# Performance work log

Hardware: AMD Instinct MI355X
Metric: run time of the kernel (lower is better)

The kernel has to match this reference:

```python
import jax, jax.numpy as jnp
import numpy as np

# QMon (monDEQ, Winston & Kolter): conv pre-net -> MONSingleConv + MONBorderReLU solved
# with Peaceman-Rachford splitting -> border crop -> MLP head.
BATCH = 256
C = 64            # DEQ channels
N = 9             # DEQ spatial dim (in_dim=9)
K = 3             # MONSingleConv kernel size
M_STRONG = 0.1    # m (strong monotonicity)
ALPHA = 1.0
TOL = 1e-5
MAX_ITER = 50
OUT_FEATURES = 18


def conv2d(x, w, b=None, stride=1):
    y = jax.lax.conv_general_dilated(x, w, (stride, stride), 'VALID',
                                     dimension_numbers=('NCHW', 'OIHW', 'NCHW'))
    if b is not None:
        y = y + b[None, :, None, None]
    return y


def circ_conv(x, w, b=None):
    # circular-padded 'same' conv (cpad + valid conv in the torch code)
    p = (w.shape[2] - 1) // 2
    xp = jnp.pad(x, ((0, 0), (0, 0), (p, p), (p, p)), mode='wrap')
    return conv2d(xp, w, b)


def circ_conv_T(x, w):
    # adjoint of circular conv = circular conv with spatially-flipped, channel-transposed kernel
    wt = jnp.transpose(jnp.flip(w, (2, 3)), (1, 0, 2, 3))
    return circ_conv(x, wt)


def W_multiply(z, A_w, g):
    # W z = (1-m) z - g * A^T A z, with A Frobenius-normalized
    An = A_w / jnp.linalg.norm(A_w)
    Az = circ_conv(z, An)
    ATAz = circ_conv_T(Az, An)
    return (1.0 - M_STRONG) * z - g * ATAz


def build_inverse(A_w, g, n):
    # ((1+alpha) I - alpha W)^{-1} per 2D-DFT frequency (circular conv is block-circulant)
    An = A_w / jnp.linalg.norm(A_w)
    co, ci, k, _ = An.shape
    p = (k - 1) // 2
    kimg = jnp.zeros((co, ci, n, n), An.dtype)
    for dx in range(k):
        for dy in range(k):
            kimg = kimg.at[:, :, (dx - p) % n, (dy - p) % n].set(An[:, :, dx, dy])
    Af = jnp.conj(jnp.fft.fft2(kimg)).transpose(2, 3, 0, 1)  # (n,n,O,I): A_hat(w)
    I = jnp.eye(co, dtype=Af.dtype)
    c = (1.0 + ALPHA) - ALPHA * (1.0 - M_STRONG)
    Mmat = c * I + (ALPHA * g).astype(Af.dtype) * jnp.einsum('xyoi,xyoj->xyij', jnp.conj(Af), Af)
    return jnp.linalg.inv(Mmat)  # (n,n,C,C) complex


def apply_inverse(Vinv, z):
    zf = jnp.fft.fft2(z)                                  # (B,C,n,n)
    yf = jnp.einsum('xyoc,bcxy->boxy', Vinv, zf)
    return jnp.real(jnp.fft.ifft2(yf)).astype(z.dtype)


def mon_deq(xpre, U_w, U_b, A_w, g):
    n = xpre.shape[-1]
    bias = circ_conv(xpre, U_w, U_b)
    Vinv = build_inverse(A_w, g, n)
    mask = jnp.pad(jnp.ones((n - 2, n - 2), xpre.dtype), 1)[None, None]  # MONBorderReLU border=1
    brelu = lambda v: jax.nn.relu(v) * mask
    z0 = jnp.zeros_like(bias)

    def body(state):
        z, u, err, it = state
        u12 = 2.0 * z - u
        z12 = apply_inverse(Vinv, u12 + ALPHA * bias)
        un = 2.0 * z12 - u12
        zn = brelu(un)
        err = jnp.linalg.norm(zn - z) / (1e-6 + jnp.linalg.norm(zn))
        return zn, un, err, it + 1

    def cond(state):
        _, _, err, it = state
        return (err > TOL) & (it < MAX_ITER)

    z, u, err, it = jax.lax.while_loop(cond, body, (z0, z0, jnp.asarray(1.0, xpre.dtype), 0))
    # final pass with the linear operator (as in the torch forward after the no_grad solve)
    return brelu(W_multiply(z, A_w, g) + bias)


def setup_inputs() -> dict:
    key = jax.random.key(0)
    ks = jax.random.split(key, 12)

    def u(k, shape, fan_in):
        b = 1.0 / np.sqrt(fan_in)
        return jax.random.uniform(k, shape, jnp.float32, -b, b)

    x = jax.random.uniform(ks[0], (BATCH, 4, 84, 84), jnp.float32) * 255.0
    return dict(
        x=x,
        conv1_w=u(ks[1], (32, 4, 8, 8), 4 * 8 * 8), conv1_b=u(ks[2], (32,), 4 * 8 * 8),
        conv2_w=u(ks[3], (64, 32, 4, 4), 32 * 4 * 4), conv2_b=u(ks[4], (64,), 32 * 4 * 4),
        U_w=u(ks[5], (C, C, K, K), C * K * K), U_b=u(ks[6], (C,), C * K * K),
        A_w=u(ks[7], (C, C, K, K), C * K * K), g=jnp.asarray(1.0, jnp.float32),
        fc1_w=u(ks[8], (512, 3136), 3136), fc1_b=u(ks[9], (512,), 3136),
        fc2_w=u(ks[10], (OUT_FEATURES, 512), 512), fc2_b=u(ks[11], (OUT_FEATURES,), 512),
    )


def reference(x, conv1_w, conv1_b, conv2_w, conv2_b, U_w, U_b, A_w, g,
              fc1_w, fc1_b, fc2_w, fc2_b):
    h = jax.nn.relu(conv2d(x / 255.0, conv1_w, conv1_b, stride=4))   # (B,32,20,20)
    h = jax.nn.relu(conv2d(h, conv2_w, conv2_b, stride=2))           # (B,64,9,9)
    z = mon_deq(h, U_w, U_b, A_w, g)                                 # (B,64,9,9)
    z = z[:, :, 1:-1, 1:-1].reshape(z.shape[0], -1)                  # (B,3136)
    h = jax.nn.relu(z @ fc1_w.T + fc1_b)
    return h @ fc2_w.T + fc2_b
```

## Files before the change

### kernel.cpp

```cpp
#include <hip/hip_runtime.h>


#define NB 256
#define NCH 64
#define NP 81
#define NIMG (NB*NCH)
#define MAXIT 50
#define NCAN 41
__device__ __host__ inline int CAN2(int l) {
    return (l < 5) ? l*9 : ((l-5)%9)*9 + ((l-5)/9 + 1);
}

constexpr float C9[9] = {
  1.0f, 0.76604444311897803f, 0.17364817766693041f, -0.5f,
  -0.93969262078590843f, -0.93969262078590843f, -0.5f,
  0.17364817766693041f, 0.76604444311897803f };
constexpr float S9[9] = {
  0.0f, 0.64278760968653936f, 0.98480775301220802f, 0.86602540378443871f,
  0.34202014332566877f, -0.34202014332566877f, -0.86602540378443871f,
  -0.98480775301220802f, -0.64278760968653936f };

__constant__ float COS9[9] = {
  1.0f, 0.76604444311897803f, 0.17364817766693041f, -0.5f,
  -0.93969262078590843f, -0.93969262078590843f, -0.5f,
  0.17364817766693041f, 0.76604444311897803f };
__constant__ float SIN9[9] = {
  0.0f, 0.64278760968653936f, 0.98480775301220802f, 0.86602540378443871f,
  0.34202014332566877f, -0.34202014332566877f, -0.86602540378443871f,
  -0.98480775301220802f, -0.64278760968653936f };

__global__ __launch_bounds__(256) void k_norm(const float* __restrict__ Aw,
                                              float* __restrict__ sc) {
    __shared__ float red[256];
    float s = 0.f;
    for (int i = threadIdx.x; i < 64*64*9; i += 256) { float a = Aw[i]; s += a*a; }
    red[threadIdx.x] = s; __syncthreads();
    for (int w = 128; w > 0; w >>= 1) {
        if (threadIdx.x < w) red[threadIdx.x] += red[threadIdx.x + w];
        __syncthreads();
    }
    if (threadIdx.x == 0) { float n = sqrtf(red[0]); sc[0] = n; sc[1] = 1.f/n; }
}

__global__ __launch_bounds__(512, 4) void k_conv1(const float* __restrict__ x,
                                                  const float* __restrict__ w,
                                                  const float* __restrict__ bb,
                                                  float* __restrict__ y) {
    __shared__ float xl[7056];
    int blk = blockIdx.x, tid = threadIdx.x;
    int b = blk >> 1, og = (blk & 1) << 4;
    float acc[16];
    #pragma unroll
    for (int o = 0; o < 16; ++o) acc[o] = 0.f;
    int p = tid, oy = p/20, ox = p%20;
    for (int ci = 0; ci < 4; ++ci) {
        __syncthreads();
        const float4* xg = (const float4*)(x + b*28224 + ci*7056);
        for (int i = tid; i < 1764; i += 512) ((float4*)xl)[i] = xg[i];
        __syncthreads();
        if (p < 400) {
            #pragma unroll
            for (int ky = 0; ky < 8; ++ky) {
                const float* xr = xl + (oy*4+ky)*84 + ox*4;
                float4 x0 = *(const float4*)xr;
                float4 x1 = *(const float4*)(xr+4);
                const float* wr = w + og*256 + ci*64 + ky*8;
                #pragma unroll
                for (int o = 0; o < 16; ++o) {
                    const float* wo = wr + o*256;
                    acc[o] += x0.x*wo[0] + x0.y*wo[1] + x0.z*wo[2] + x0.w*wo[3]
                            + x1.x*wo[4] + x1.y*wo[5] + x1.z*wo[6] + x1.w*wo[7];
                }
            }
        }
    }
    if (p < 400) {
        #pragma unroll
        for (int o = 0; o < 16; ++o)
            y[b*12800 + (og+o)*400 + p] = fmaxf(acc[o]*(1.f/255.f) + bb[og+o], 0.f);
    }
}

__global__ __launch_bounds__(512, 2) void k_conv2(const float* __restrict__ h1,
                                                  const float* __restrict__ w2,
                                                  const float* __restrict__ b2,
                                                  float* __restrict__ h2) {
    int blk = blockIdx.x, tid = threadIdx.x;
    int b = blk >> 2, og = (blk & 3) << 4;
    __shared__ float hl[16*400];
    __shared__ float wl[16*512];
    for (int i = tid; i < 8192; i += 512) wl[i] = w2[og*512 + i];
    float a0[2], a1[2];
    #pragma unroll
    for (int s = 0; s < 2; ++s) { a0[s] = 0.f; a1[s] = 0.f; }
    for (int cp = 0; cp < 2; ++cp) {
        __syncthreads();
        for (int i = tid; i < 6400; i += 512) {
            int ci = i / 400, pix = i % 400, iy = pix / 20, ix = pix % 20;
            hl[ci*400 + ((iy&1)*2 + (ix&1))*100 + (iy>>1)*10 + (ix>>1)]
                = h1[b*12800 + (cp*16 + ci)*400 + pix];
        }
        __syncthreads();
        #pragma unroll
        for (int s = 0; s < 2; ++s) {
            int idx = tid + s*512;
            if (idx < 648) {
                int op = idx/81, p = idx%81;
                int oy = p/9, ox = p%9;
                int toff[16];
                #pragma unroll
                for (int ky = 0; ky < 4; ky++)
                #pragma unroll
                for (int kx = 0; kx < 4; kx++)
                    toff[ky*4+kx] = ((ky&1)*2 + (kx&1))*100
                                  + (oy + (ky>>1))*10 + (ox + (kx>>1));
                const float* w0 = wl + op*2*512 + cp*256;
                for (int ci = 0; ci < 16; ci++) {
                    float t[16];
                    const float* base = hl + ci*400;
                    #pragma unroll
                    for (int q = 0; q < 16; ++q) t[q] = base[toff[q]];
                    const float* wb0 = w0 + ci*16;
                    const float* wb1 = w0 + 512 + ci*16;
                    #pragma unroll
                    for (int q = 0; q < 16; ++q) {
                        a0[s] += t[q]*wb0[q]; a1[s] += t[q]*wb1[q];
                    }
                }
            }
        }
    }
    #pragma unroll
    for (int s = 0; s < 2; ++s) {
        int idx = tid + s*512;
        if (idx < 648) {
            int op = idx/81, p = idx%81;
            int o = og + op*2;
            h2[b*5184 + o*81 + p]     = fmaxf(a0[s] + b2[o],   0.f);
            h2[b*5184 + (o+1)*81 + p] = fmaxf(a1[s] + b2[o+1], 0.f);
        }
    }
}

__global__ __launch_bounds__(512, 2) void k_bias(const float* __restrict__ h2,
                                                 const float* __restrict__ Uw,
                                                 const float* __restrict__ Ub,
                                                 float* __restrict__ biasT) {
    int blk = blockIdx.x, tid = threadIdx.x;
    int b = blk >> 2, og = (blk & 3) << 4;
    __shared__ float h2l[5184];
    __shared__ float wl[16*576];
    __shared__ float bt[1296];
    for (int i = tid; i < 5184; i += 512) h2l[i] = h2[b*5184 + i];
    for (int i = tid; i < 9216; i += 512) wl[i] = Uw[og*576 + i];
    __syncthreads();
    for (int idx = tid; idx < 648; idx += 512) {
        int op = idx/81, p = idx%81;
        int i0 = p/9, j0 = p%9;
        int im = (i0+8)%9, ip = (i0+1)%9, jm = (j0+8)%9, jp = (j0+1)%9;
        int toff[9] = { im*9+jm, im*9+j0, im*9+jp,
                        i0*9+jm, i0*9+j0, i0*9+jp,
                        ip*9+jm, ip*9+j0, ip*9+jp };
        float a0 = 0.f, a1 = 0.f;
        const float* w0 = wl + op*2*576;
        for (int ci = 0; ci < 64; ci++) {
            float t[9];
            const float* hb = h2l + ci*81;
            #pragma unroll
            for (int q = 0; q < 9; ++q) t[q] = hb[toff[q]];
            const float* wb0 = w0 + ci*9;
            const float* wb1 = w0 + 576 + ci*9;
            #pragma unroll
            for (int q = 0; q < 9; ++q) { a0 += t[q]*wb0[q]; a1 += t[q]*wb1[q]; }
        }
        bt[(op*2)*81 + p]   = a0 + Ub[og + op*2];
        bt[(op*2+1)*81 + p] = a1 + Ub[og + op*2 + 1];
    }
    __syncthreads();
    for (int idx = tid; idx < 1296; idx += 512) {
        int p2 = idx >> 4, o16 = idx & 15;
        biasT[p2*NIMG + b*64 + og + o16] = bt[o16*81 + p2];
    }
}

__global__ __launch_bounds__(256) void k_af(const float* __restrict__ Aw,
                                            const float* __restrict__ sc,
                                            float2* __restrict__ Af) {
    int l = blockIdx.x; int f = CAN2(l);
    int x = f/9, y = f%9;
    float inv = sc[1];
    for (int pr = threadIdx.x; pr < 4096; pr += 256) {
        const float* a = Aw + pr*9;
        float re = 0.f, im = 0.f;
        #pragma unroll
        for (int dx = 0; dx < 3; dx++)
        #pragma unroll
        for (int dy = 0; dy < 3; dy++) {
            int tt = (x*(dx+8) + y*(dy+8)) % 9;
            float v = a[dx*3+dy] * inv;
            re += v * COS9[tt]; im += v * SIN9[tt];
        }
        Af[f*4096 + pr] = make_float2(re, im);
    }
}

__global__ __launch_bounds__(256) void k_mw(const float2* __restrict__ Af,
                                            const float* __restrict__ gp,
                                            float2* __restrict__ Mmat,
                                            float2* __restrict__ WmT) {
    int l = blockIdx.x >> 2, q = blockIdx.x & 3;
    int f = CAN2(l);
    float g = gp[0];
    __shared__ float2 Al[4096];
    for (int i = threadIdx.x; i < 4096; i += 256) Al[i] = Af[f*4096 + i];
    __syncthreads();
    int e = q*1024 + threadIdx.x;
    #pragma unroll
    for (int rep = 0; rep < 4; ++rep, e += 256) {
        int i = e >> 6, j = e & 63;
        float sr = 0.f, si = 0.f;
        for (int o = 0; o < 64; o++) {
            float2 a = Al[o*64 + i], b = Al[o*64 + j];
            sr += a.x*b.x + a.y*b.y;
            si += a.x*b.y - a.y*b.x;
        }
        Mmat[f*4096 + e] = make_float2((i==j ? 1.1f : 0.f) + g*sr, g*si);
        WmT [f*4096 + j*64 + i] = make_float2((i==j ? 0.9f : 0.f) - g*sr, -g*si);
    }
}

__global__ __launch_bounds__(512, 1) void k_inv(float2* __restrict__ Mio) {
    int f = CAN2((int)blockIdx.x);
    __shared__ float2 Mt[64*65];
    __shared__ float2 rowk[2][64];
    __shared__ float2 fcol[2][64];
    int tid = threadIdx.x;
    int i = tid & 63, jg = tid >> 6;
    float2* Mg = Mio + f*4096;
    for (int e = tid; e < 4096; e += 512) Mt[(e>>6)*65 + (e&63)] = Mg[e];
    __syncthreads();
    float2 r[8];
    #pragma unroll
    for (int jj = 0; jj < 8; ++jj) r[jj] = Mt[i*65 + jg*8 + jj];

    for (int k = 0; k < 64; ++k) {
        int buf = k & 1;
        if (i == k) {
            #pragma unroll
            for (int jj = 0; jj < 8; ++jj) rowk[buf][jg*8 + jj] = r[jj];
        }
        if (jg == (k >> 3)) {
            int sel = k & 7;
            float2 v = r[0];
            #pragma unroll
            for (int jj = 1; jj < 8; ++jj) v = (sel == jj) ? r[jj] : v;
            fcol[buf][i] = v;
        }
        __syncthreads();
        float2 d = rowk[buf][k];
        float den = 1.f / (d.x*d.x + d.y*d.y);
        float pr = d.x*den, pi = -d.y*den;
        float2 fi = fcol[buf][i];
        bool piv = (i == k);
        #pragma unroll
        for (int jj = 0; jj < 8; ++jj) {
            int j = jg*8 + jj;
            float2 rw = rowk[buf][j];
            float2 rkj = (j == k) ? make_float2(pr, pi)
                                  : make_float2(rw.x*pr - rw.y*pi,
                                                rw.x*pi + rw.y*pr);
            if (piv) {
                r[jj] = rkj;
            } else {
                float bx = (j == k) ? 0.f : r[jj].x;
                float by = (j == k) ? 0.f : r[jj].y;
                r[jj] = make_float2(bx - (fi.x*rkj.x - fi.y*rkj.y),
                                    by - (fi.x*rkj.y + fi.y*rkj.x));
            }
        }
    }
    __syncthreads();
    #pragma unroll
    for (int jj = 0; jj < 8; ++jj) Mt[(jg*8 + jj)*65 + i] = r[jj];
    __syncthreads();
    for (int e = tid; e < 4096; e += 512) Mg[e] = Mt[(e>>6)*65 + (e&63)];
}

__global__ __launch_bounds__(320) void k_fft(const float* __restrict__ biasT,
                                             float2* __restrict__ Tf) {
    __shared__ float2 T1[9*5*64];
    int lane = threadIdx.x & 63, j = threadIdx.x >> 6;
    int gimg = blockIdx.x*64 + lane;
    for (int r = j; r < 9; r += 5) {
        float tn[9];
        #pragma unroll
        for (int xc = 0; xc < 9; ++xc) tn[xc] = biasT[(r*9 + xc)*NIMG + gimg];
        #pragma unroll
        for (int ky = 0; ky < 5; ++ky) {
            float sr = 0.f, si = 0.f;
            #pragma unroll
            for (int xx = 0; xx < 9; ++xx) {
                const int m = (ky*xx) % 9;
                sr += tn[xx]*C9[m];
                si -= tn[xx]*S9[m];
            }
            T1[(r*5 + ky)*64 + lane] = make_float2(sr, si);
        }
    }
    __syncthreads();
    {
        int ky = j;
        float2 s[9];
        #pragma unroll
        for (int r = 0; r < 9; ++r) s[r] = T1[(r*5 + ky)*64 + lane];
        #pragma unroll
        for (int kx = 0; kx < 9; ++kx) {
            if (kx < 5 || ky > 0) {
                float fr = 0.f, fi = 0.f;
                #pragma unroll
                for (int r = 0; r < 9; ++r) {
                    const int m = (kx*r) % 9;
                    fr += s[r].x*C9[m] + s[r].y*S9[m];
                    fi += s[r].y*C9[m] - s[r].x*S9[m];
                }
                Tf[(kx*9 + ky)*NIMG + gimg] = make_float2(fr, fi);
            }
        }
    }
}

__global__ __launch_bounds__(256) void k_mv(const float2* __restrict__ Tf,
                                            float2* __restrict__ Yf,
                                            const float2* __restrict__ V) {
    int l = blockIdx.x >> 4, bc = blockIdx.x & 15;
    int f = CAN2(l);
    int lane = threadIdx.x & 63;
    int wid  = __builtin_amdgcn_readfirstlane((int)(threadIdx.x >> 6));
    int b0 = bc*16 + wid*4;
    const float2* Vg = V + f*4096 + lane;
    const float2* Tg = Tf + f*NIMG + b0*64;
    float2 a0 = make_float2(0.f,0.f), a1 = a0, a2 = a0, a3 = a0;
    #pragma unroll 8
    for (int c = 0; c < 64; ++c) {
        float2 v = Vg[c*64];
        float2 t0 = Tg[c], t1 = Tg[64+c], t2 = Tg[128+c], t3 = Tg[192+c];
        a0.x += v.x*t0.x - v.y*t0.y; a0.y += v.x*t0.y + v.y*t0.x;
        a1.x += v.x*t1.x - v.y*t1.y; a1.y += v.x*t1.y + v.y*t1.x;
        a2.x += v.x*t2.x - v.y*t2.y; a2.y += v.x*t2.y + v.y*t2.x;
        a3.x += v.x*t3.x - v.y*t3.y; a3.y += v.x*t3.y + v.y*t3.x;
    }
    float2* Yg = Yf + f*NIMG + b0*64 + lane;
    Yg[0] = a0; Yg[64] = a1; Yg[128] = a2; Yg[192] = a3;
}

__global__ __launch_bounds__(640) void k_fuse(const float2* __restrict__ Yf,
                                              float* __restrict__ u12T,
                                              const float* __restrict__ biasT,
                                              float2* __restrict__ Tf,
                                              int last) {
    __shared__ float2 T1[9*5*64];
    int lane = threadIdx.x & 63, j = threadIdx.x >> 6;
    int gimg = blockIdx.x*64 + lane;
    {
        int ky = j >> 1;
        float2 y[9];
        #pragma unroll
        for (int kx = 0; kx < 9; ++kx) {
            int fc; bool cj;
            if (ky == 0 && kx >= 5) { fc = (9 - kx)*9; cj = true; }
            else                    { fc = kx*9 + ky;  cj = false; }
            float2 a = Yf[fc*NIMG + gimg];
            y[kx] = make_float2(a.x, cj ? -a.y : a.y);
        }
        if ((j & 1) == 0) {
            #pragma unroll
            for (int r = 0; r < 5; ++r) {
                float sr = 0.f, si = 0.f;
                #pragma unroll
                for (int kx = 0; kx < 9; ++kx) {
                    const int m = (r*kx) % 9;
                    sr += y[kx].x*C9[m] - y[kx].y*S9[m];
                    si += y[kx].x*S9[m] + y[kx].y*C9[m];
                }
                T1[(r*5 + ky)*64 + lane] = make_float2(sr, si);
            }
        } else {
            #pragma unroll
            for (int r = 5; r < 9; ++r) {
                float sr = 0.f, si = 0.f;
                #pragma unroll
                for (int kx = 0; kx < 9; ++kx) {
                    const int m = (r*kx) % 9;
                    sr += y[kx].x*C9[m] - y[kx].y*S9[m];
                    si += y[kx].x*S9[m] + y[kx].y*C9[m];
                }
                T1[(r*5 + ky)*64 + lane] = make_float2(sr, si);
            }
        }
    }
    __syncthreads();
    if (j < 9) {
        int r = j;
        float2 t1[5];
        #pragma unroll
        for (int ky = 0; ky < 5; ++ky) t1[ky] = T1[(r*5 + ky)*64 + lane];
        float tn[9];
        #pragma unroll
        for (int xc = 0; xc < 9; ++xc) {
            float yr = t1[0].x;
            #pragma unroll
            for (int ky = 1; ky < 5; ++ky) {
                const int m = (xc*ky) % 9;
                yr += 2.f*(t1[ky].x*C9[m] - t1[ky].y*S9[m]);
            }
            yr *= (1.f/81.f);
            int gi = (r*9 + xc)*NIMG + gimg;
            float u12v = u12T[gi];
            float un = 2.f*yr - u12v;
            bool interior = (r >= 1 && r <= 7 && xc >= 1 && xc <= 7);
            float zn = interior ? fmaxf(un, 0.f) : 0.f;
            float u12n = 2.f*zn - un;
            u12T[gi] = u12n;
            tn[xc] = last ? zn : (u12n + biasT[gi]);
        }
        #pragma unroll
        for (int ky = 0; ky < 5; ++ky) {
            float sr = 0.f, si = 0.f;
            #pragma unroll
            for (int xx = 0; xx < 9; ++xx) {
                const int m = (ky*xx) % 9;
                sr += tn[xx]*C9[m];
                si -= tn[xx]*S9[m];
            }
            T1[(r*5 + ky)*64 + lane] = make_float2(sr, si);
        }
    }
    __syncthreads();
    {
        int ky = j >> 1;
        float2 s[9];
        #pragma unroll
        for (int rr = 0; rr < 9; ++rr) s[rr] = T1[(rr*5 + ky)*64 + lane];
        if ((j & 1) == 0) {
            #pragma unroll
            for (int kx = 0; kx < 5; ++kx) {
                float fr = 0.f, fi = 0.f;
                #pragma unroll
                for (int rr = 0; rr < 9; ++rr) {
                    const int m = (kx*rr) % 9;
                    fr += s[rr].x*C9[m] + s[rr].y*S9[m];
                    fi += s[rr].y*C9[m] - s[rr].x*S9[m];
                }
                Tf[(kx*9 + ky)*NIMG + gimg] = make_float2(fr, fi);
            }
        } else if (ky > 0) {
            #pragma unroll
            for (int kx = 5; kx < 9; ++kx) {
                float fr = 0.f, fi = 0.f;
                #pragma unroll
                for (int rr = 0; rr < 9; ++rr) {
                    const int m = (kx*rr) % 9;
                    fr += s[rr].x*C9[m] + s[rr].y*S9[m];
                    fi += s[rr].y*C9[m] - s[rr].x*S9[m];
                }
                Tf[(kx*9 + ky)*NIMG + gimg] = make_float2(fr, fi);
            }
        }
    }
}

__global__ __launch_bounds__(320) void k_crop(const float2* __restrict__ Yf,
                                              const float* __restrict__ biasT,
                                              float* __restrict__ zc) {
    __shared__ float2 T1[9*5*64];
    int lane = threadIdx.x & 63, j = threadIdx.x >> 6;
    int gimg = blockIdx.x*64 + lane;
    {
        int ky = j;
        float2 y[9];
        #pragma unroll
        for (int kx = 0; kx < 9; ++kx) {
            int fc; bool cj;
            if (ky == 0 && kx >= 5) { fc = (9 - kx)*9; cj = true; }
            else                    { fc = kx*9 + ky;  cj = false; }
            float2 a = Yf[fc*NIMG + gimg];
            y[kx] = make_float2(a.x, cj ? -a.y : a.y);
        }
        #pragma unroll
        for (int r = 0; r < 9; ++r) {
            float sr = 0.f, si = 0.f;
            #pragma unroll
            for (int kx = 0; kx < 9; ++kx) {
                const int m = (r*kx) % 9;
                sr += y[kx].x*C9[m] - y[kx].y*S9[m];
                si += y[kx].x*S9[m] + y[kx].y*C9[m];
            }
            T1[(r*5 + ky)*64 + lane] = make_float2(sr, si);
        }
    }
    __syncthreads();
    for (int r = 1 + j; r <= 7; r += 5) {
        float2 t1[5];
        #pragma unroll
        for (int ky = 0; ky < 5; ++ky) t1[ky] = T1[(r*5 + ky)*64 + lane];
        float* zr = zc + (gimg >> 6)*3136 + (gimg & 63)*49 + (r-1)*7;
        #pragma unroll
        for (int xc = 1; xc < 8; ++xc) {
            float yr = t1[0].x;
            #pragma unroll
            for (int ky = 1; ky < 5; ++ky) {
                const int m = (xc*ky) % 9;
                yr += 2.f*(t1[ky].x*C9[m] - t1[ky].y*S9[m]);
            }
            yr *= (1.f/81.f);
            zr[xc-1] = fmaxf(yr + biasT[(r*9 + xc)*NIMG + gimg], 0.f);
        }
    }
}

__global__ __launch_bounds__(256) void k_fc1(const float* __restrict__ A,
                                             const float* __restrict__ W,
                                             const float* __restrict__ bb,
                                             float* __restrict__ H) {
    int bt = blockIdx.x >> 5, ot = blockIdx.x & 31;
    int b0 = bt*16, o0 = ot*16;
    __shared__ float At[16][65], Bt[16][65];
    int tid = threadIdx.x;
    int row = tid >> 6, col = tid & 63;
    int tb = tid >> 4, to = tid & 15;
    float acc = 0.f;
    for (int k0 = 0; k0 < 3136; k0 += 64) {
        #pragma unroll
        for (int s = 0; s < 4; s++) {
            int rr = row + s*4;
            At[rr][col] = A[(b0+rr)*3136 + k0 + col];
            Bt[rr][col] = W[(o0+rr)*3136 + k0 + col];
        }
        __syncthreads();
        #pragma unroll
        for (int kk = 0; kk < 64; kk++)
            acc += At[tb][kk] * Bt[to][kk];
        __syncthreads();
    }
    H[(b0+tb)*512 + o0+to] = fmaxf(acc + bb[o0+to], 0.f);
}

__global__ __launch_bounds__(256) void k_fc2(const float* __restrict__ H,
                                             const float* __restrict__ W,
                                             const float* __restrict__ bb,
                                             float* __restrict__ out) {
    int idx = blockIdx.x*256 + threadIdx.x;
    if (idx >= 4608) return;
    int b = idx/18, o = idx%18;
    const float* h = H + b*512;
    const float* w = W + o*512;
    float acc = 0.f;
    for (int k = 0; k < 512; k++) acc += h[k]*w[k];
    out[idx] = acc + bb[o];
}

extern "C" void kernel_launch(void* const* d_in, const int* in_sizes, int n_in,
                              void* d_out, int out_size, void* d_ws, size_t ws_size,
                              hipStream_t stream) {
    (void)in_sizes; (void)n_in; (void)out_size; (void)ws_size;
    const float* x   = (const float*)d_in[0];
    const float* c1w = (const float*)d_in[1];
    const float* c1b = (const float*)d_in[2];
    const float* c2w = (const float*)d_in[3];
    const float* c2b = (const float*)d_in[4];
    const float* Uw  = (const float*)d_in[5];
    const float* Ub  = (const float*)d_in[6];
    const float* Aw  = (const float*)d_in[7];
    const float* gp  = (const float*)d_in[8];
    const float* f1w = (const float*)d_in[9];
    const float* f1b = (const float*)d_in[10];
    const float* f2w = (const float*)d_in[11];
    const float* f2b = (const float*)d_in[12];

    float* ws = (float*)d_ws;
    float*  h1    = ws + 0;
    float2* Tf    = (float2*)(ws + 0);
    float*  biasT = ws + 3276800;
    float*  u12T  = ws + 4603904;
    float2* Yf    = (float2*)(ws + 5931008);
    float2* Af    = (float2*)(ws + 8585216);
    float2* Minv  = (float2*)(ws + 9248768);
    float2* WmT   = (float2*)(ws + 9912320);
    float*  zc    = ws + 10575872;
    float*  hfc   = ws + 11378688;
    float*  sc    = ws + 11509760;
    float*  h2    = ws + 11509764;

    hipMemsetAsync(u12T, 0, (size_t)1327104*sizeof(float), stream);

    k_norm <<<1,     256, 0, stream>>>(Aw, sc);
    k_conv1<<<512,   512, 0, stream>>>(x, c1w, c1b, h1);
    k_conv2<<<1024,  512, 0, stream>>>(h1, c2w, c2b, h2);
    k_bias <<<1024,  512, 0, stream>>>(h2, Uw, Ub, biasT);
    k_af   <<<NCAN,  256, 0, stream>>>(Aw, sc, Af);
    k_mw   <<<NCAN*4,256, 0, stream>>>(Af, gp, Minv, WmT);
    k_inv  <<<NCAN,  512, 0, stream>>>(Minv);

    k_fft<<<256, 320, 0, stream>>>(biasT, Tf);
    for (int it = 0; it < MAXIT; it++) {
        k_mv  <<<NCAN*16, 256, 0, stream>>>(Tf, Yf, Minv);
        k_fuse<<<256,     640, 0, stream>>>(Yf, u12T, biasT, Tf, it == MAXIT-1);
    }
    k_mv  <<<NCAN*16, 256, 0, stream>>>(Tf, Yf, WmT);
    k_crop<<<256,     320, 0, stream>>>(Yf, biasT, zc);

    k_fc1<<<512, 256, 0, stream>>>(zc, f1w, f1b, hfc);
    k_fc2<<<18,  256, 0, stream>>>(hfc, f2w, f2b, (float*)d_out);
}
```

Measured before the change: 1.720 ms.

## Fuse FFT, per-frequency matvec, IFFT and update into one iteration kernel

Each Peaceman-Rachford iteration now runs in a single kernel per 64-image block: forward 2D DFT, per-frequency 64x64 complex matvec against the inverse matrices, inverse DFT, and the ReLU splitting update all go through shared memory. The global Tf/Yf spectral buffers and the separate mv/fft/crop launches are removed, and the final W multiply and crop are folded into the last iteration. This cuts global traffic for the frequency-domain intermediates and halves launch count. The trade-off is that each block now rereads all 41 frequency matrices (about 2.6 MB) from global/L2 every iteration. The matvec also processes only one image per lane-group instead of reusing V across 4 images, and uses fewer blocks (256) with heavy shared memory.

```diff
diff --git a/kernel.cpp b/kernel.cpp
--- a/kernel.cpp
+++ b/kernel.cpp
@@ -286,125 +286,132 @@
     for (int e = tid; e < 4096; e += 512) Mg[e] = Mt[(e>>6)*65 + (e&63)];
 }
 
-__global__ __launch_bounds__(320) void k_fft(const float* __restrict__ biasT,
-                                             float2* __restrict__ Tf) {
-    __shared__ float2 T1[9*5*64];
+__device__ __forceinline__ void fft_st1(const float* tn, float2* bufA,
+                                        int lane, int r) {
+    #pragma unroll
+    for (int ky = 0; ky < 5; ++ky) {
+        float sr = 0.f, si = 0.f;
+        #pragma unroll
+        for (int xx = 0; xx < 9; ++xx) {
+            const int m = (ky*xx) % 9;
+            sr += tn[xx]*C9[m];
+            si -= tn[xx]*S9[m];
+        }
+        bufA[(r*5 + ky)*64 + lane] = make_float2(sr, si);
+    }
+}
+
+__device__ __forceinline__ void fft_st2(const float2* bufA, float2* bufT,
+                                        int lane, int j) {
+    int ky = j >> 1;
+    float2 s[9];
+    #pragma unroll
+    for (int rr = 0; rr < 9; ++rr) s[rr] = bufA[(rr*5 + ky)*64 + lane];
+    if ((j & 1) == 0) {
+        #pragma unroll
+        for (int kx = 0; kx < 5; ++kx) {
+            float fr = 0.f, fi = 0.f;
+            #pragma unroll
+            for (int rr = 0; rr < 9; ++rr) {
+                const int m = (kx*rr) % 9;
+                fr += s[rr].x*C9[m] + s[rr].y*S9[m];
+                fi += s[rr].y*C9[m] - s[rr].x*S9[m];
+            }
+            int l = (ky == 0) ? kx : 5 + (ky-1)*9 + kx;
+            bufT[l*64 + lane] = make_float2(fr, fi);
+        }
+    } else if (ky > 0) {
+        #pragma unroll
+        for (int kx = 5; kx < 9; ++kx) {
+            float fr = 0.f, fi = 0.f;
+            #pragma unroll
+            for (int rr = 0; rr < 9; ++rr) {
+                const int m = (kx*rr) % 9;
+                fr += s[rr].x*C9[m] + s[rr].y*S9[m];
+                fi += s[rr].y*C9[m] - s[rr].x*S9[m];
+            }
+            int l = 5 + (ky-1)*9 + kx;
+            bufT[l*64 + lane] = make_float2(fr, fi);
+        }
+    }
+}
+
+__device__ __forceinline__ void mv_phase(const float2* __restrict__ V,
+                                         const float2* bufT, float2* bufY,
+                                         int lane, int j) {
+    for (int l = j; l < NCAN; l += 10) {
+        const float2* Vg = V + CAN2(l)*4096 + lane;
+        float2 a = make_float2(0.f, 0.f);
+        #pragma unroll 8
+        for (int c = 0; c < 64; ++c) {
+            float2 v = Vg[c*64];
+            float2 t = bufT[l*64 + c];
+            a.x += v.x*t.x - v.y*t.y;
+            a.y += v.x*t.y + v.y*t.x;
+        }
+        bufY[l*64 + lane] = a;
+    }
+}
+
+__device__ __forceinline__ void ifft_st1(const float2* bufY, float2* bufW,
+                                         int lane, int j) {
+    int ky = j >> 1;
+    float2 y[9];
+    #pragma unroll
+    for (int kx = 0; kx < 9; ++kx) {
+        int l; bool cj;
+        if (ky == 0 && kx >= 5) { l = 9 - kx; cj = true; }
+        else { l = (ky == 0) ? kx : 5 + (ky-1)*9 + kx; cj = false; }
+        float2 a = bufY[l*64 + lane];
+        y[kx] = make_float2(a.x, cj ? -a.y : a.y);
+    }
+    int r0 = (j & 1) ? 5 : 0, r1 = (j & 1) ? 9 : 5;
+    for (int r = r0; r < r1; ++r) {
+        float sr = 0.f, si = 0.f;
+        #pragma unroll
+        for (int kx = 0; kx < 9; ++kx) {
+            const int m = (r*kx) % 9;
+            sr += y[kx].x*C9[m] - y[kx].y*S9[m];
+            si += y[kx].x*S9[m] + y[kx].y*C9[m];
+        }
+        bufW[(r*5 + ky)*64 + lane] = make_float2(sr, si);
+    }
+}
+
+__global__ __launch_bounds__(640) void k_iter(float* __restrict__ u12T,
+                                              const float* __restrict__ biasT,
+                                              const float2* __restrict__ Vm,
+                                              const float2* __restrict__ Wm,
+                                              float* __restrict__ zc,
+                                              int last) {
+    __shared__ float2 bufA[2880];
+    __shared__ float2 bufB[2880];
     int lane = threadIdx.x & 63, j = threadIdx.x >> 6;
     int gimg = blockIdx.x*64 + lane;
-    for (int r = j; r < 9; r += 5) {
-        float tn[9];
-        #pragma unroll
-        for (int xc = 0; xc < 9; ++xc) tn[xc] = biasT[(r*9 + xc)*NIMG + gimg];
-        #pragma unroll
-        for (int ky = 0; ky < 5; ++ky) {
-            float sr = 0.f, si = 0.f;
-            #pragma unroll
-            for (int xx = 0; xx < 9; ++xx) {
-                const int m = (ky*xx) % 9;
-                sr += tn[xx]*C9[m];
-                si -= tn[xx]*S9[m];
-            }
-            T1[(r*5 + ky)*64 + lane] = make_float2(sr, si);
-        }
-    }
-    __syncthreads();
-    {
-        int ky = j;
-        float2 s[9];
-        #pragma unroll
-        for (int r = 0; r < 9; ++r) s[r] = T1[(r*5 + ky)*64 + lane];
-        #pragma unroll
-        for (int kx = 0; kx < 9; ++kx) {
-            if (kx < 5 || ky > 0) {
-                float fr = 0.f, fi = 0.f;
-                #pragma unroll
-                for (int r = 0; r < 9; ++r) {
-                    const int m = (kx*r) % 9;
-                    fr += s[r].x*C9[m] + s[r].y*S9[m];
-                    fi += s[r].y*C9[m] - s[r].x*S9[m];
-                }
-                Tf[(kx*9 + ky)*NIMG + gimg] = make_float2(fr, fi);
-            }
-        }
-    }
-}
-
-__global__ __launch_bounds__(256) void k_mv(const float2* __restrict__ Tf,
-                                            float2* __restrict__ Yf,
-                                            const float2* __restrict__ V) {
-    int l = blockIdx.x >> 4, bc = blockIdx.x & 15;
-    int f = CAN2(l);
-    int lane = threadIdx.x & 63;
-    int wid  = __builtin_amdgcn_readfirstlane((int)(threadIdx.x >> 6));
-    int b0 = bc*16 + wid*4;
-    const float2* Vg = V + f*4096 + lane;
-    const float2* Tg = Tf + f*NIMG + b0*64;
-    float2 a0 = make_float2(0.f,0.f), a1 = a0, a2 = a0, a3 = a0;
-    #pragma unroll 8
-    for (int c = 0; c < 64; ++c) {
-        float2 v = Vg[c*64];
-        float2 t0 = Tg[c], t1 = Tg[64+c], t2 = Tg[128+c], t3 = Tg[192+c];
-        a0.x += v.x*t0.x - v.y*t0.y; a0.y += v.x*t0.y + v.y*t0.x;
-        a1.x += v.x*t1.x - v.y*t1.y; a1.y += v.x*t1.y + v.y*t1.x;
-        a2.x += v.x*t2.x - v.y*t2.y; a2.y += v.x*t2.y + v.y*t2.x;
-        a3.x += v.x*t3.x - v.y*t3.y; a3.y += v.x*t3.y + v.y*t3.x;
-    }
-    float2* Yg = Yf + f*NIMG + b0*64 + lane;
-    Yg[0] = a0; Yg[64] = a1; Yg[128] = a2; Yg[192] = a3;
-}
-
-__global__ __launch_bounds__(640) void k_fuse(const float2* __restrict__ Yf,
-                                              float* __restrict__ u12T,
-                                              const float* __restrict__ biasT,
-                                              float2* __restrict__ Tf,
-                                              int last) {
-    __shared__ float2 T1[9*5*64];
-    int lane = threadIdx.x & 63, j = threadIdx.x >> 6;
-    int gimg = blockIdx.x*64 + lane;
-    {
-        int ky = j >> 1;
-        float2 y[9];
-        #pragma unroll
-        for (int kx = 0; kx < 9; ++kx) {
-            int fc; bool cj;
-            if (ky == 0 && kx >= 5) { fc = (9 - kx)*9; cj = true; }
-            else                    { fc = kx*9 + ky;  cj = false; }
-            float2 a = Yf[fc*NIMG + gimg];
-            y[kx] = make_float2(a.x, cj ? -a.y : a.y);
-        }
-        if ((j & 1) == 0) {
-            #pragma unroll
-            for (int r = 0; r < 5; ++r) {
-                float sr = 0.f, si = 0.f;
-                #pragma unroll
-                for (int kx = 0; kx < 9; ++kx) {
-                    const int m = (r*kx) % 9;
-                    sr += y[kx].x*C9[m] - y[kx].y*S9[m];
-                    si += y[kx].x*S9[m] + y[kx].y*C9[m];
-                }
-                T1[(r*5 + ky)*64 + lane] = make_float2(sr, si);
-            }
-        } else {
-            #pragma unroll
-            for (int r = 5; r < 9; ++r) {
-                float sr = 0.f, si = 0.f;
-                #pragma unroll
-                for (int kx = 0; kx < 9; ++kx) {
-                    const int m = (r*kx) % 9;
-                    sr += y[kx].x*C9[m] - y[kx].y*S9[m];
-                    si += y[kx].x*S9[m] + y[kx].y*C9[m];
-                }
-                T1[(r*5 + ky)*64 + lane] = make_float2(sr, si);
-            }
-        }
-    }
+    float u12v[9], bv[9], tn[9];
+    if (j < 9) {
+        int r = j;
+        #pragma unroll
+        for (int xc = 0; xc < 9; ++xc) {
+            int gi = (r*9 + xc)*NIMG + gimg;
+            u12v[xc] = u12T[gi];
+            bv[xc]   = biasT[gi];
+            tn[xc]   = u12v[xc] + bv[xc];
+        }
+        fft_st1(tn, bufA, lane, r);
+    }
+    __syncthreads();
+    fft_st2(bufA, bufB, lane, j);
+    __syncthreads();
+    mv_phase(Vm, bufB, bufA, lane, j);
+    __syncthreads();
+    ifft_st1(bufA, bufB, lane, j);
     __syncthreads();
     if (j < 9) {
         int r = j;
         float2 t1[5];
         #pragma unroll
-        for (int ky = 0; ky < 5; ++ky) t1[ky] = T1[(r*5 + ky)*64 + lane];
-        float tn[9];
+        for (int ky = 0; ky < 5; ++ky) t1[ky] = bufB[(r*5 + ky)*64 + lane];
         #pragma unroll
         for (int xc = 0; xc < 9; ++xc) {
             float yr = t1[0].x;
@@ -414,95 +421,29 @@
                 yr += 2.f*(t1[ky].x*C9[m] - t1[ky].y*S9[m]);
             }
             yr *= (1.f/81.f);
-            int gi = (r*9 + xc)*NIMG + gimg;
-            float u12v = u12T[gi];
-            float un = 2.f*yr - u12v;
+            float un = 2.f*yr - u12v[xc];
             bool interior = (r >= 1 && r <= 7 && xc >= 1 && xc <= 7);
             float zn = interior ? fmaxf(un, 0.f) : 0.f;
             float u12n = 2.f*zn - un;
-            u12T[gi] = u12n;
-            tn[xc] = last ? zn : (u12n + biasT[gi]);
-        }
-        #pragma unroll
-        for (int ky = 0; ky < 5; ++ky) {
-            float sr = 0.f, si = 0.f;
-            #pragma unroll
-            for (int xx = 0; xx < 9; ++xx) {
-                const int m = (ky*xx) % 9;
-                sr += tn[xx]*C9[m];
-                si -= tn[xx]*S9[m];
-            }
-            T1[(r*5 + ky)*64 + lane] = make_float2(sr, si);
-        }
-    }
-    __syncthreads();
-    {
-        int ky = j >> 1;
-        float2 s[9];
-        #pragma unroll
-        for (int rr = 0; rr < 9; ++rr) s[rr] = T1[(rr*5 + ky)*64 + lane];
-        if ((j & 1) == 0) {
-            #pragma unroll
-            for (int kx = 0; kx < 5; ++kx) {
-                float fr = 0.f, fi = 0.f;
-                #pragma unroll
-                for (int rr = 0; rr < 9; ++rr) {
-                    const int m = (kx*rr) % 9;
-                    fr += s[rr].x*C9[m] + s[rr].y*S9[m];
-                    fi += s[rr].y*C9[m] - s[rr].x*S9[m];
-                }
-                Tf[(kx*9 + ky)*NIMG + gimg] = make_float2(fr, fi);
-            }
-        } else if (ky > 0) {
-            #pragma unroll
-            for (int kx = 5; kx < 9; ++kx) {
-                float fr = 0.f, fi = 0.f;
-                #pragma unroll
-                for (int rr = 0; rr < 9; ++rr) {
-                    const int m = (kx*rr) % 9;
-                    fr += s[rr].x*C9[m] + s[rr].y*S9[m];
-                    fi += s[rr].y*C9[m] - s[rr].x*S9[m];
-                }
-                Tf[(kx*9 + ky)*NIMG + gimg] = make_float2(fr, fi);
-            }
-        }
-    }
-}
-
-__global__ __launch_bounds__(320) void k_crop(const float2* __restrict__ Yf,
-                                              const float* __restrict__ biasT,
-                                              float* __restrict__ zc) {
-    __shared__ float2 T1[9*5*64];
-    int lane = threadIdx.x & 63, j = threadIdx.x >> 6;
-    int gimg = blockIdx.x*64 + lane;
-    {
-        int ky = j;
-        float2 y[9];
-        #pragma unroll
-        for (int kx = 0; kx < 9; ++kx) {
-            int fc; bool cj;
-            if (ky == 0 && kx >= 5) { fc = (9 - kx)*9; cj = true; }
-            else                    { fc = kx*9 + ky;  cj = false; }
-            float2 a = Yf[fc*NIMG + gimg];
-            y[kx] = make_float2(a.x, cj ? -a.y : a.y);
-        }
-        #pragma unroll
-        for (int r = 0; r < 9; ++r) {
-            float sr = 0.f, si = 0.f;
-            #pragma unroll
-            for (int kx = 0; kx < 9; ++kx) {
-                const int m = (r*kx) % 9;
-                sr += y[kx].x*C9[m] - y[kx].y*S9[m];
-                si += y[kx].x*S9[m] + y[kx].y*C9[m];
-            }
-            T1[(r*5 + ky)*64 + lane] = make_float2(sr, si);
-        }
-    }
-    __syncthreads();
-    for (int r = 1 + j; r <= 7; r += 5) {
+            u12T[(r*9 + xc)*NIMG + gimg] = u12n;
+            tn[xc] = zn;
+        }
+    }
+    if (!last) return;
+    __syncthreads();
+    if (j < 9) fft_st1(tn, bufA, lane, j);
+    __syncthreads();
+    fft_st2(bufA, bufB, lane, j);
+    __syncthreads();
+    mv_phase(Wm, bufB, bufA, lane, j);
+    __syncthreads();
+    ifft_st1(bufA, bufB, lane, j);
+    __syncthreads();
+    if (j >= 1 && j <= 7) {
+        int r = j;
         float2 t1[5];
         #pragma unroll
-        for (int ky = 0; ky < 5; ++ky) t1[ky] = T1[(r*5 + ky)*64 + lane];
+        for (int ky = 0; ky < 5; ++ky) t1[ky] = bufB[(r*5 + ky)*64 + lane];
         float* zr = zc + (gimg >> 6)*3136 + (gimg & 63)*49 + (r-1)*7;
         #pragma unroll
         for (int xc = 1; xc < 8; ++xc) {
@@ -513,7 +454,7 @@
                 yr += 2.f*(t1[ky].x*C9[m] - t1[ky].y*S9[m]);
             }
             yr *= (1.f/81.f);
-            zr[xc-1] = fmaxf(yr + biasT[(r*9 + xc)*NIMG + gimg], 0.f);
+            zr[xc-1] = fmaxf(yr + bv[xc], 0.f);
         }
     }
 }
@@ -579,17 +520,15 @@
 
     float* ws = (float*)d_ws;
     float*  h1    = ws + 0;
-    float2* Tf    = (float2*)(ws + 0);
     float*  biasT = ws + 3276800;
     float*  u12T  = ws + 4603904;
-    float2* Yf    = (float2*)(ws + 5931008);
-    float2* Af    = (float2*)(ws + 8585216);
-    float2* Minv  = (float2*)(ws + 9248768);
-    float2* WmT   = (float2*)(ws + 9912320);
-    float*  zc    = ws + 10575872;
-    float*  hfc   = ws + 11378688;
-    float*  sc    = ws + 11509760;
-    float*  h2    = ws + 11509764;
+    float2* Af    = (float2*)(ws + 5931008);
+    float2* Minv  = (float2*)(ws + 6594560);
+    float2* WmT   = (float2*)(ws + 7258112);
+    float*  zc    = ws + 7921664;
+    float*  hfc   = ws + 8724480;
+    float*  sc    = ws + 8855552;
+    float*  h2    = ws + 8855556;
 
     hipMemsetAsync(u12T, 0, (size_t)1327104*sizeof(float), stream);
 
@@ -601,13 +540,9 @@
     k_mw   <<<NCAN*4,256, 0, stream>>>(Af, gp, Minv, WmT);
     k_inv  <<<NCAN,  512, 0, stream>>>(Minv);
 
-    k_fft<<<256, 320, 0, stream>>>(biasT, Tf);
-    for (int it = 0; it < MAXIT; it++) {
-        k_mv  <<<NCAN*16, 256, 0, stream>>>(Tf, Yf, Minv);
-        k_fuse<<<256,     640, 0, stream>>>(Yf, u12T, biasT, Tf, it == MAXIT-1);
-    }
-    k_mv  <<<NCAN*16, 256, 0, stream>>>(Tf, Yf, WmT);
-    k_crop<<<256,     320, 0, stream>>>(Yf, biasT, zc);
+    for (int it = 0; it < MAXIT; it++)
+        k_iter<<<256, 640, 0, stream>>>(u12T, biasT, Minv, WmT, zc,
+                                        it == MAXIT-1);
 
     k_fc1<<<512, 256, 0, stream>>>(zc, f1w, f1b, hfc);
     k_fc2<<<18,  256, 0, stream>>>(hfc, f2w, f2b, (float*)d_out);
```

Measured after the change: 1.931 ms. +12.2%, slower.
